# Kernel tuning notes

Measured on AMD Instinct MI355X. Metric: run time of the kernel, lower is better.

The kernel has to match this reference:

```python
import jax, jax.numpy as jnp
import numpy as np

TOP_K = 5
EPS = 1e-12  # torch F.normalize eps


def l2norm(x, axis=-1):
    n = jnp.sqrt(jnp.sum(x * x, axis=axis, keepdims=True))
    return x / jnp.maximum(n, EPS)


def setup_inputs() -> dict:
    key = jax.random.key(0)
    k1, k2, k3, k4 = jax.random.split(key, 4)
    B, L, P, Lp, D = 1024, 12, 100, 8, 768
    return {
        "x_query": jax.random.normal(k1, (B, L, D), dtype=jnp.float32),
        "K_all": jax.random.normal(k2, (L, P, D), dtype=jnp.float32),
        "A_all": jax.random.normal(k3, (L, P, D), dtype=jnp.float32),
        "P_all": jax.random.normal(k4, (L, P, Lp, D), dtype=jnp.float32),
    }


def reference(x_query, K_all, A_all, P_all):
    # Inference path (train=False) of L2PppMaskAttn.forward.
    # x_query: [B, L, D]; K_all/A_all: [L, P, D]; P_all: [L, P, Lp, E]
    q = jax.lax.stop_gradient(l2norm(x_query))  # query is .detach()ed in the original
    q = jnp.swapaxes(q, 0, 1)  # [L, B, D]

    def per_layer(q_l, K, A, Pp):
        n_K = l2norm(K)                              # [P, D]
        cos_sim = jnp.einsum('bj,kj->bk', q_l, n_K)  # [B, P]
        _, k_idx = jax.lax.top_k(cos_sim, TOP_K)     # [B, top_k]
        Kg = K[k_idx]                                # [B, k, D]
        Ag = A[k_idx]                                # [B, k, D]
        Pg = Pp[k_idx]                               # [B, k, Lp, E]
        a_k = jnp.sum(l2norm(Kg) * l2norm(Ag), axis=-1)  # [B, k]
        return jnp.einsum('bk,bkle->ble', a_k, Pg)   # [B, Lp, E]

    p_return = jax.vmap(per_layer)(q, K_all, A_all, P_all)  # [L, B, Lp, E]
    return p_return
```

## Files before the change

kernel.cpp:

```cpp
#include <hip/hip_runtime.h>
#include <cstdint>

#define L_NUM 12
#define B_NUM 1024
#define P_NUM 100
#define LP_NUM 8
#define D_NUM 768
#define TILE_E (LP_NUM * D_NUM)
#define TOPK 5
#define GQ 8
#define EPSF 1e-12f

__device__ __forceinline__ unsigned long long makeKey(float f, int p) {
    union { float f; uint32_t u; } v; v.f = f;
    uint32_t u = v.u;
    u = (u & 0x80000000u) ? ~u : (u | 0x80000000u);
    return ((unsigned long long)u << 32) | (unsigned)(127 - p);
}

__global__ __launch_bounds__(64) void proto_stats_kernel(
    const float* __restrict__ K, const float* __restrict__ A,
    float* __restrict__ invK, float* __restrict__ sArr)
{
    const int lp = blockIdx.x;
    const int lane = threadIdx.x;
    const float4* Kp = (const float4*)(K + (size_t)lp * D_NUM);
    const float4* Ap = (const float4*)(A + (size_t)lp * D_NUM);
    float kk = 0.f, aa = 0.f, ka = 0.f;
#pragma unroll
    for (int c = 0; c < 3; c++) {
        float4 k4 = Kp[c * 64 + lane];
        float4 a4 = Ap[c * 64 + lane];
        kk += k4.x * k4.x + k4.y * k4.y + k4.z * k4.z + k4.w * k4.w;
        aa += a4.x * a4.x + a4.y * a4.y + a4.z * a4.z + a4.w * a4.w;
        ka += k4.x * a4.x + k4.y * a4.y + k4.z * a4.z + k4.w * a4.w;
    }
#pragma unroll
    for (int off = 32; off; off >>= 1) {
        kk += __shfl_xor(kk, off);
        aa += __shfl_xor(aa, off);
        ka += __shfl_xor(ka, off);
    }
    if (lane == 0) {
        float nk = fmaxf(sqrtf(kk), EPSF);
        float na = fmaxf(sqrtf(aa), EPSF);
        invK[lp] = 1.0f / nk;
        sArr[lp] = ka / (nk * na);
    }
}

__global__ __launch_bounds__(256) void scores_top5_kernel(
    const float* __restrict__ X,
    const float* __restrict__ K,
    const float* __restrict__ invK,
    const float* __restrict__ sArr,
    int*   __restrict__ topIdx,
    float* __restrict__ topW)
{
    const int b0 = blockIdx.x * GQ;
    const int l  = blockIdx.y;
    const int tid = threadIdx.x;
    const int lane = tid & 63;
    const int w = tid >> 6;

    __shared__ float sc[GQ][P_NUM];

    float4 q[GQ][3];
#pragma unroll
    for (int g = 0; g < GQ; g++) {
        const float4* Q = (const float4*)(X + ((size_t)(b0 + g) * L_NUM + l) * D_NUM);
#pragma unroll
        for (int c = 0; c < 3; c++) q[g][c] = Q[c * 64 + lane];
    }

    for (int i = 0; i < 25; i++) {
        const int p = w * 25 + i;
        const float4* Kp = (const float4*)(K + ((size_t)l * P_NUM + p) * D_NUM);
        float4 kv0 = Kp[0 * 64 + lane];
        float4 kv1 = Kp[1 * 64 + lane];
        float4 kv2 = Kp[2 * 64 + lane];
        float acc[GQ];
#pragma unroll
        for (int g = 0; g < GQ; g++) {
            acc[g] = q[g][0].x * kv0.x + q[g][0].y * kv0.y + q[g][0].z * kv0.z + q[g][0].w * kv0.w
                   + q[g][1].x * kv1.x + q[g][1].y * kv1.y + q[g][1].z * kv1.z + q[g][1].w * kv1.w
                   + q[g][2].x * kv2.x + q[g][2].y * kv2.y + q[g][2].z * kv2.z + q[g][2].w * kv2.w;
        }
#pragma unroll
        for (int off = 32; off; off >>= 1) {
#pragma unroll
            for (int g = 0; g < GQ; g++) acc[g] += __shfl_xor(acc[g], off);
        }
        if (lane == 0) {
            const float s = invK[l * P_NUM + p];
#pragma unroll
            for (int g = 0; g < GQ; g++) sc[g][p] = acc[g] * s;
        }
    }
    __syncthreads();

#pragma unroll
    for (int pass = 0; pass < 2; pass++) {
        const int g = w + pass * 4;
        float s0 = sc[g][lane];
        float s1 = (lane + 64 < P_NUM) ? sc[g][lane + 64] : -3.0e38f;
        unsigned long long k0 = makeKey(s0, lane);
        unsigned long long k1 = makeKey(s1, lane + 64);
        const size_t base = ((size_t)l * B_NUM + (b0 + g)) * TOPK;
        for (int j = 0; j < TOPK; j++) {
            unsigned long long m = k0 > k1 ? k0 : k1;
#pragma unroll
            for (int off = 32; off; off >>= 1) {
                unsigned long long o = __shfl_xor(m, off);
                if (o > m) m = o;
            }
            if (k0 == m) k0 = 0ull;
            if (k1 == m) k1 = 0ull;
            if (lane == 0) {
                int p = 127 - (int)(m & 127ull);
                topIdx[base + j] = p;
                topW[base + j]   = sArr[l * P_NUM + p];
            }
        }
    }
}

__global__ __launch_bounds__(256) void gather_out_kernel(
    const float* __restrict__ Pall,
    const int*   __restrict__ topIdx,
    const float* __restrict__ topW,
    float* __restrict__ out)
{
    const int b = blockIdx.x;
    const int l = blockIdx.y;
    const int tid = threadIdx.x;
    const size_t lb = (size_t)l * B_NUM + b;

    int   pk[TOPK];
    float wk[TOPK];
#pragma unroll
    for (int j = 0; j < TOPK; j++) {
        pk[j] = topIdx[lb * TOPK + j];
        wk[j] = topW[lb * TOPK + j];
    }

    const float* Pl = Pall + (size_t)l * P_NUM * TILE_E;
    const float4* Pr[TOPK];
#pragma unroll
    for (int j = 0; j < TOPK; j++) Pr[j] = (const float4*)(Pl + (size_t)pk[j] * TILE_E);

    float4* outv = (float4*)(out + lb * TILE_E);

#pragma unroll
    for (int it = 0; it < 6; it++) {
        const int e4 = it * 256 + tid;
        float4 r = make_float4(0.f, 0.f, 0.f, 0.f);
#pragma unroll
        for (int j = 0; j < TOPK; j++) {
            const float4 pu = Pr[j][e4];
            const float wj = wk[j];
            r.x += wj * pu.x; r.y += wj * pu.y; r.z += wj * pu.z; r.w += wj * pu.w;
        }
        outv[e4] = r;
    }
}

extern "C" void kernel_launch(void* const* d_in, const int* in_sizes, int n_in,
                              void* d_out, int out_size, void* d_ws, size_t ws_size,
                              hipStream_t stream) {
    const float* X  = (const float*)d_in[0];
    const float* K  = (const float*)d_in[1];
    const float* A  = (const float*)d_in[2];
    const float* Pp = (const float*)d_in[3];

    float* invK  = (float*)d_ws;
    float* sArr  = invK + L_NUM * P_NUM;
    int*   topIdx = (int*)(sArr + L_NUM * P_NUM);
    float* topW  = (float*)(topIdx + L_NUM * B_NUM * TOPK);

    proto_stats_kernel<<<L_NUM * P_NUM, 64, 0, stream>>>(K, A, invK, sArr);
    scores_top5_kernel<<<dim3(B_NUM / GQ, L_NUM), 256, 0, stream>>>(
        X, K, invK, sArr, topIdx, topW);
    gather_out_kernel<<<dim3(B_NUM, L_NUM), 256, 0, stream>>>(
        Pp, topIdx, topW, (float*)d_out);
}
```

Before: 493.1 us.

## Fuse top-k selection with prompt gather into a single kernel

Merges the scoring/top-5 kernel and the gather-weighted-sum kernel so each block keeps its selected indices and weights in shared memory and writes the output for its 8 queries directly. This removes one launch and the global round trip for the top-k indices and weights. In exchange the gather phase now runs with only 1536 blocks, each doing 8 sequential output tiles, instead of 12288 independent blocks, which cuts parallelism for the bandwidth-bound output write.

```diff
diff --git a/kernel.cpp b/kernel.cpp
--- a/kernel.cpp
+++ b/kernel.cpp
@@ -49,13 +49,13 @@
     }
 }
 
-__global__ __launch_bounds__(256) void scores_top5_kernel(
+__global__ __launch_bounds__(256) void fused_main_kernel(
     const float* __restrict__ X,
     const float* __restrict__ K,
+    const float* __restrict__ Pall,
     const float* __restrict__ invK,
     const float* __restrict__ sArr,
-    int*   __restrict__ topIdx,
-    float* __restrict__ topW)
+    float* __restrict__ out)
 {
     const int b0 = blockIdx.x * GQ;
     const int l  = blockIdx.y;
@@ -64,6 +64,8 @@
     const int w = tid >> 6;
 
     __shared__ float sc[GQ][P_NUM];
+    __shared__ int   idx_s[GQ][TOPK];
+    __shared__ float wgt_s[GQ][TOPK];
 
     float4 q[GQ][3];
 #pragma unroll
@@ -106,7 +108,6 @@
         float s1 = (lane + 64 < P_NUM) ? sc[g][lane + 64] : -3.0e38f;
         unsigned long long k0 = makeKey(s0, lane);
         unsigned long long k1 = makeKey(s1, lane + 64);
-        const size_t base = ((size_t)l * B_NUM + (b0 + g)) * TOPK;
         for (int j = 0; j < TOPK; j++) {
             unsigned long long m = k0 > k1 ? k0 : k1;
 #pragma unroll
@@ -118,50 +119,36 @@
             if (k1 == m) k1 = 0ull;
             if (lane == 0) {
                 int p = 127 - (int)(m & 127ull);
-                topIdx[base + j] = p;
-                topW[base + j]   = sArr[l * P_NUM + p];
+                idx_s[g][j] = p;
+                wgt_s[g][j] = sArr[l * P_NUM + p];
             }
         }
     }
-}
-
-__global__ __launch_bounds__(256) void gather_out_kernel(
-    const float* __restrict__ Pall,
-    const int*   __restrict__ topIdx,
-    const float* __restrict__ topW,
-    float* __restrict__ out)
-{
-    const int b = blockIdx.x;
-    const int l = blockIdx.y;
-    const int tid = threadIdx.x;
-    const size_t lb = (size_t)l * B_NUM + b;
-
-    int   pk[TOPK];
-    float wk[TOPK];
-#pragma unroll
-    for (int j = 0; j < TOPK; j++) {
-        pk[j] = topIdx[lb * TOPK + j];
-        wk[j] = topW[lb * TOPK + j];
-    }
+    __syncthreads();
 
     const float* Pl = Pall + (size_t)l * P_NUM * TILE_E;
-    const float4* Pr[TOPK];
 #pragma unroll
-    for (int j = 0; j < TOPK; j++) Pr[j] = (const float4*)(Pl + (size_t)pk[j] * TILE_E);
-
-    float4* outv = (float4*)(out + lb * TILE_E);
-
-#pragma unroll
-    for (int it = 0; it < 6; it++) {
-        const int e4 = it * 256 + tid;
-        float4 r = make_float4(0.f, 0.f, 0.f, 0.f);
+    for (int g = 0; g < GQ; g++) {
+        const float4* Pr[TOPK];
+        float wk[TOPK];
 #pragma unroll
         for (int j = 0; j < TOPK; j++) {
-            const float4 pu = Pr[j][e4];
-            const float wj = wk[j];
-            r.x += wj * pu.x; r.y += wj * pu.y; r.z += wj * pu.z; r.w += wj * pu.w;
+            Pr[j] = (const float4*)(Pl + (size_t)idx_s[g][j] * TILE_E);
+            wk[j] = wgt_s[g][j];
         }
-        outv[e4] = r;
+        float4* outv = (float4*)(out + ((size_t)l * B_NUM + (b0 + g)) * TILE_E);
+#pragma unroll
+        for (int it = 0; it < 6; it++) {
+            const int e4 = it * 256 + tid;
+            float4 r = make_float4(0.f, 0.f, 0.f, 0.f);
+#pragma unroll
+            for (int j = 0; j < TOPK; j++) {
+                const float4 pu = Pr[j][e4];
+                const float wj = wk[j];
+                r.x += wj * pu.x; r.y += wj * pu.y; r.z += wj * pu.z; r.w += wj * pu.w;
+            }
+            outv[e4] = r;
+        }
     }
 }
 
@@ -173,14 +160,10 @@
     const float* A  = (const float*)d_in[2];
     const float* Pp = (const float*)d_in[3];
 
-    float* invK  = (float*)d_ws;
-    float* sArr  = invK + L_NUM * P_NUM;
-    int*   topIdx = (int*)(sArr + L_NUM * P_NUM);
-    float* topW  = (float*)(topIdx + L_NUM * B_NUM * TOPK);
+    float* invK = (float*)d_ws;
+    float* sArr = invK + L_NUM * P_NUM;
 
     proto_stats_kernel<<<L_NUM * P_NUM, 64, 0, stream>>>(K, A, invK, sArr);
-    scores_top5_kernel<<<dim3(B_NUM / GQ, L_NUM), 256, 0, stream>>>(
-        X, K, invK, sArr, topIdx, topW);
-    gather_out_kernel<<<dim3(B_NUM, L_NUM), 256, 0, stream>>>(
-        Pp, topIdx, topW, (float*)d_out);
+    fused_main_kernel<<<dim3(B_NUM / GQ, L_NUM), 256, 0, stream>>>(
+        X, K, Pp, invK, sArr, (float*)d_out);
 }
```

Result: faster. 478.7 us (-2.9%).
